# Kernel tuning notes

Hardware: AMD Instinct MI355X
Metric: run time of the kernel (lower is better)

Reference implementation:

```python
import jax, jax.numpy as jnp
import numpy as np


def _conv1x1(x, w, b):
    # x: [B,C,H,W], w: [O,C], b: [O] -> [B,O,H,W]
    return jnp.einsum('bchw,oc->bohw', x, w) + b[None, :, None, None]


def setup_inputs() -> dict:
    key = jax.random.key(0)
    ks = jax.random.split(key, 5)
    B, C, H, W = 4, 256, 64, 64
    C2 = C // 2
    scale = 0.02  # keep attention logits in a sane range
    return {
        'x': jax.random.normal(ks[0], (B, C, H, W), dtype=jnp.float32),
        'w_theta': jax.random.normal(ks[1], (C2, C), dtype=jnp.float32) * scale,
        'b_theta': jnp.zeros((C2,), dtype=jnp.float32),
        'w_phi': jax.random.normal(ks[2], (C2, C), dtype=jnp.float32) * scale,
        'b_phi': jnp.zeros((C2,), dtype=jnp.float32),
        'w_g': jax.random.normal(ks[3], (C2, C), dtype=jnp.float32) * scale,
        'b_g': jnp.zeros((C2,), dtype=jnp.float32),
        'w_out': jax.random.normal(ks[4], (C, C2), dtype=jnp.float32) * scale,
        'b_out': jnp.zeros((C,), dtype=jnp.float32),
    }


def reference(x, w_theta, b_theta, w_phi, b_phi, w_g, b_g, w_out, b_out):
    B, C, H, W = x.shape
    C2 = C // 2
    N = H * W
    theta = _conv1x1(x, w_theta, b_theta).reshape(B, C2, N)  # [B,C2,N]
    phi = _conv1x1(x, w_phi, b_phi).reshape(B, C2, N)        # [B,C2,N]
    g = _conv1x1(x, w_g, b_g).reshape(B, C2, N)              # [B,C2,N]
    # non-local attention: scores[b,m,n] = theta[b,:,m] . phi[b,:,n]
    scores = jnp.einsum('bcm,bcn->bmn', theta, phi)          # [B,N,N]
    attn = jax.nn.softmax(scores, axis=-1)                   # [B,N,N]
    # output = g @ attn^T : out[b,c,m] = sum_n g[b,c,n] * attn[b,m,n]
    out = jnp.einsum('bcn,bmn->bcm', g, attn)                # [B,C2,N]
    out = out.reshape(B, C2, H, W)
    return x + _conv1x1(out, w_out, b_out)
```

## Files before the change

### kernel.cpp

```cpp
#include <hip/hip_runtime.h>
#include <hip/hip_bf16.h>

#define B_  4
#define C_  256
#define C2_ 128
#define N_  4096
#define LOG2E 1.4426950408889634f

typedef unsigned short u16;
typedef __attribute__((ext_vector_type(8))) short bf16x8;
typedef __attribute__((ext_vector_type(4))) float f32x4;

static __device__ __forceinline__ u16 f2bf(float f) {
    return __builtin_bit_cast(u16, __float2bfloat16(f));
}
static __device__ __forceinline__ float bf2f(u16 u) {
    return __bfloat162float(__builtin_bit_cast(__hip_bfloat16, u));
}
static __device__ __forceinline__ bf16x8 cvt8(const float* p) {
    u16 t[8];
#pragma unroll
    for (int j = 0; j < 8; ++j) t[j] = f2bf(p[j]);
    return *(const bf16x8*)t;
}

__global__ __launch_bounds__(256, 2) void projx_kernel(
    const float* __restrict__ x,
    const float* __restrict__ wt, const float* __restrict__ wp,
    const float* __restrict__ wg,
    const float* __restrict__ b_theta, const float* __restrict__ b_phi,
    const float* __restrict__ b_g,
    u16* __restrict__ Q, u16* __restrict__ K, u16* __restrict__ V) {
    __shared__ __align__(16) u16 XTs[64][264];
    __shared__ __align__(16) u16 Ws[64][264];
    u16 (*Vt)[72] = (u16(*)[72])XTs;

    int bid = blockIdx.x;
    int b   = bid / (N_ / 64);
    int n0  = (bid % (N_ / 64)) * 64;
    int tid = threadIdx.x;
    int wave = tid >> 6, lane = tid & 63, quad = (lane >> 4) & 3, l16 = lane & 15;

#pragma unroll
    for (int it = 0; it < 8; ++it) {
        int idx = it * 256 + tid;
        int q = idx & 15, p = idx >> 4;
        const float* r0 = x + ((size_t)b * C_ + 2 * p) * N_ + n0 + 4 * q;
        float4 v0 = *(const float4*)r0;
        float4 v1 = *(const float4*)(r0 + N_);
        const float* f0 = (const float*)&v0;
        const float* f1 = (const float*)&v1;
#pragma unroll
        for (int j = 0; j < 4; ++j) {
            unsigned pk = (unsigned)f2bf(f0[j]) | ((unsigned)f2bf(f1[j]) << 16);
            *(unsigned*)&XTs[4 * q + j][2 * p] = pk;
        }
    }
    __syncthreads();

    bf16x8 af[8];
#pragma unroll
    for (int ks = 0; ks < 8; ++ks)
        af[ks] = *(const bf16x8*)&XTs[wave * 16 + l16][ks * 32 + quad * 8];
    __syncthreads();

    const float* wms[3]    = { wt, wp, wg };
    const float* biases[3] = { b_theta, b_phi, b_g };

#pragma unroll
    for (int mat = 0; mat < 3; ++mat) {
        const float* wm = wms[mat];
        const float* bias = biases[mat];
#pragma unroll
        for (int h = 0; h < 2; ++h) {
#pragma unroll
            for (int it = 0; it < 8; ++it) {
                int idx = it * 256 + tid;
                int row = idx >> 5, c8 = (idx & 31) * 8;
                const float* src = wm + (size_t)(h * 64 + row) * C_ + c8;
                float w8[8];
                *(float4*)&w8[0] = *(const float4*)src;
                *(float4*)&w8[4] = *(const float4*)(src + 4);
                bf16x8 v = cvt8(w8);
                *(bf16x8*)&Ws[row][c8] = v;
            }
            __syncthreads();

            f32x4 acc[4];
#pragma unroll
            for (int i = 0; i < 4; ++i) acc[i] = (f32x4){0.f, 0.f, 0.f, 0.f};
#pragma unroll
            for (int ct = 0; ct < 4; ++ct)
#pragma unroll
                for (int ks = 0; ks < 8; ++ks) {
                    bf16x8 bf = *(const bf16x8*)&Ws[ct * 16 + l16][ks * 32 + quad * 8];
                    acc[ct] = __builtin_amdgcn_mfma_f32_16x16x32_bf16(
                        af[ks], bf, acc[ct], 0, 0, 0);
                }

            if (mat < 2) {
                u16* dst = mat == 0 ? Q : K;
                float sc = mat == 0 ? LOG2E : 1.0f;
#pragma unroll
                for (int ct = 0; ct < 4; ++ct) {
                    int c2 = h * 64 + ct * 16 + l16;
                    float bb = bias[c2];
#pragma unroll
                    for (int r = 0; r < 4; ++r) {
                        int n = n0 + wave * 16 + quad * 4 + r;
                        dst[((size_t)b * N_ + n) * C2_ + c2] =
                            f2bf((acc[ct][r] + bb) * sc);
                    }
                }
            } else {
#pragma unroll
                for (int ct = 0; ct < 4; ++ct) {
                    int c2 = h * 64 + ct * 16 + l16;
                    float bb = bias[c2];
#pragma unroll
                    for (int r = 0; r < 4; ++r)
                        Vt[c2][wave * 16 + quad * 4 + r] = f2bf(acc[ct][r] + bb);
                }
            }
            __syncthreads();
        }
    }

#pragma unroll
    for (int it = 0; it < 4; ++it) {
        int idx = it * 256 + tid;
        int row = idx >> 3, n8 = (idx & 7) * 8;
        *(uint4*)(V + ((size_t)b * C2_ + row) * N_ + n0 + n8) =
            *(const uint4*)&Vt[row][n8];
    }
}

__global__ __launch_bounds__(256, 2) void attn_kernel(
    const u16* __restrict__ Q, const u16* __restrict__ K,
    const u16* __restrict__ V, u16* __restrict__ AO,
    u16* __restrict__ Opb, float* __restrict__ lsum, int nsplit) {
    const int BM = 128, BN = 64, D = C2_;
    const int per = B_ * (N_ / BM);
    int s    = blockIdx.x / per;
    int r0   = blockIdx.x % per;
    int b    = r0 / (N_ / BM);
    int m0   = (r0 % (N_ / BM)) * BM;
    int tid  = threadIdx.x;
    int wave = tid >> 6, lane = tid & 63, quad = (lane >> 4) & 3, l16 = lane & 15;

    __shared__ __align__(16) u16 Ks[BN][D + 8];
    __shared__ __align__(16) u16 Vs[D][BN + 8];
    __shared__ __align__(16) u16 Psb[4][32][BN + 8];
    u16* Ps = &Psb[wave][0][0];

    bf16x8 qf[2][4];
#pragma unroll
    for (int ms = 0; ms < 2; ++ms) {
        const u16* qp = Q + ((size_t)b * N_ + m0 + wave * 32 + ms * 16 + l16) * D;
#pragma unroll
        for (int kk = 0; kk < 4; ++kk)
            qf[ms][kk] = *(const bf16x8*)(qp + kk * 32 + quad * 8);
    }

    float l_r[2][4] = {{0.f, 0.f, 0.f, 0.f}, {0.f, 0.f, 0.f, 0.f}};
    f32x4 o_acc[2][8];
#pragma unroll
    for (int ms = 0; ms < 2; ++ms)
#pragma unroll
        for (int i = 0; i < 8; ++i) o_acc[ms][i] = (f32x4){0.f, 0.f, 0.f, 0.f};

    const int tiles = N_ / BN;
    const int base = tiles / nsplit, rem = tiles % nsplit;
    const int t0 = s * base + (s < rem ? s : rem);
    const int cnt = base + (s < rem ? 1 : 0);
    const int nt0 = t0 * BN, nt1 = (t0 + cnt) * BN;

    for (int nt = nt0; nt < nt1; nt += BN) {
        const u16* kp = K + ((size_t)b * N_ + nt) * D;
#pragma unroll
        for (int it = 0; it < 4; ++it) {
            int idx = it * 256 + tid;
            int row = idx >> 4, col = (idx & 15) * 8;
            *(uint4*)&Ks[row][col] = *(const uint4*)(kp + row * D + col);
        }
#pragma unroll
        for (int it = 0; it < 4; ++it) {
            int idx = it * 256 + tid;
            int row = idx >> 3, col = (idx & 7) * 8;
            *(uint4*)&Vs[row][col] =
                *(const uint4*)(V + ((size_t)b * C2_ + row) * N_ + nt + col);
        }
        __syncthreads();

        f32x4 sc[2][4];
#pragma unroll
        for (int nn = 0; nn < 4; ++nn) {
            f32x4 a0 = (f32x4){0.f, 0.f, 0.f, 0.f};
            f32x4 a1 = (f32x4){0.f, 0.f, 0.f, 0.f};
#pragma unroll
            for (int kk = 0; kk < 4; ++kk) {
                bf16x8 kf = *(const bf16x8*)&Ks[nn * 16 + l16][kk * 32 + quad * 8];
                a0 = __builtin_amdgcn_mfma_f32_16x16x32_bf16(qf[0][kk], kf, a0, 0, 0, 0);
                a1 = __builtin_amdgcn_mfma_f32_16x16x32_bf16(qf[1][kk], kf, a1, 0, 0, 0);
            }
            sc[0][nn] = a0;
            sc[1][nn] = a1;
        }

#pragma unroll
        for (int ms = 0; ms < 2; ++ms)
#pragma unroll
            for (int nn = 0; nn < 4; ++nn)
#pragma unroll
                for (int r = 0; r < 4; ++r) {
                    float p = __builtin_amdgcn_exp2f(sc[ms][nn][r]);
                    l_r[ms][r] += p;
                    Ps[(ms * 16 + quad * 4 + r) * (BN + 8) + nn * 16 + l16] = f2bf(p);
                }

#pragma unroll
        for (int ks = 0; ks < 2; ++ks) {
            bf16x8 pf0 = *(const bf16x8*)&Ps[(l16) * (BN + 8) + ks * 32 + quad * 8];
            bf16x8 pf1 = *(const bf16x8*)&Ps[(16 + l16) * (BN + 8) + ks * 32 + quad * 8];
#pragma unroll
            for (int cs = 0; cs < 8; ++cs) {
                bf16x8 vf = *(const bf16x8*)&Vs[cs * 16 + l16][ks * 32 + quad * 8];
                o_acc[0][cs] = __builtin_amdgcn_mfma_f32_16x16x32_bf16(pf0, vf, o_acc[0][cs], 0, 0, 0);
                o_acc[1][cs] = __builtin_amdgcn_mfma_f32_16x16x32_bf16(pf1, vf, o_acc[1][cs], 0, 0, 0);
            }
        }
        __syncthreads();
    }

#pragma unroll
    for (int ms = 0; ms < 2; ++ms)
#pragma unroll
        for (int r = 0; r < 4; ++r) {
            l_r[ms][r] += __shfl_xor(l_r[ms][r], 1);
            l_r[ms][r] += __shfl_xor(l_r[ms][r], 2);
            l_r[ms][r] += __shfl_xor(l_r[ms][r], 4);
            l_r[ms][r] += __shfl_xor(l_r[ms][r], 8);
        }

    if (Opb) {
#pragma unroll
        for (int ms = 0; ms < 2; ++ms) {
#pragma unroll
            for (int cs = 0; cs < 8; ++cs)
#pragma unroll
                for (int r = 0; r < 4; ++r) {
                    size_t row = (size_t)s * (B_ * N_) + (size_t)b * N_ +
                                 m0 + wave * 32 + ms * 16 + quad * 4 + r;
                    Opb[row * C2_ + cs * 16 + l16] = f2bf(o_acc[ms][cs][r]);
                }
            if (l16 == 0)
#pragma unroll
                for (int r = 0; r < 4; ++r) {
                    size_t row = (size_t)s * (B_ * N_) + (size_t)b * N_ +
                                 m0 + wave * 32 + ms * 16 + quad * 4 + r;
                    lsum[row] = l_r[ms][r];
                }
        }
    } else {
#pragma unroll
        for (int ms = 0; ms < 2; ++ms)
#pragma unroll
            for (int cs = 0; cs < 8; ++cs)
#pragma unroll
                for (int r = 0; r < 4; ++r) {
                    float v = o_acc[ms][cs][r] / l_r[ms][r];
                    AO[((size_t)b * N_ + m0 + wave * 32 + ms * 16 + quad * 4 + r) * C2_ +
                       cs * 16 + l16] = f2bf(v);
                }
    }
}

__global__ __launch_bounds__(256) void outproj_kernel(
    const float* __restrict__ x, const u16* __restrict__ Opb,
    const float* __restrict__ lsum, const u16* __restrict__ AO,
    const float* __restrict__ w_out, const float* __restrict__ b_out,
    float* __restrict__ y, int nsplit) {
    __shared__ __align__(16) u16 As[64][C2_ + 8];
    __shared__ __align__(16) u16 Ws2[64][C2_ + 8];
    __shared__ float Ls[64];
    int bid = blockIdx.x;
    int per_b = (C_ / 64) * (N_ / 64);
    int b   = bid / per_b;
    int rem = bid % per_b;
    int c0  = (rem / (N_ / 64)) * 64;
    int n0  = (rem % (N_ / 64)) * 64;
    int tid = threadIdx.x;
    int wave = tid >> 6, lane = tid & 63, quad = (lane >> 4) & 3, l16 = lane & 15;

#pragma unroll
    for (int it = 0; it < 4; ++it) {
        int idx = it * 256 + tid;
        int row = idx >> 4, c8 = (idx & 15) * 8;
        const float* src = w_out + (size_t)(c0 + row) * C2_ + c8;
        float w8[8];
        *(float4*)&w8[0] = *(const float4*)src;
        *(float4*)&w8[4] = *(const float4*)(src + 4);
        bf16x8 v = cvt8(w8);
        *(bf16x8*)&Ws2[row][c8] = v;
    }

    if (nsplit > 1) {
        if (tid < 64) {
            float L = 0.f;
            for (int s = 0; s < nsplit; ++s)
                L += lsum[(size_t)s * (B_ * N_) + (size_t)b * N_ + n0 + tid];
            Ls[tid] = 1.f / L;
        }
        __syncthreads();
#pragma unroll
        for (int it = 0; it < 4; ++it) {
            int idx = it * 256 + tid;
            int n = idx >> 4, c8 = (idx & 15) * 8;
            float a[8] = {0.f, 0.f, 0.f, 0.f, 0.f, 0.f, 0.f, 0.f};
            for (int s = 0; s < nsplit; ++s) {
                const u16* op = Opb +
                    ((size_t)s * (B_ * N_) + (size_t)b * N_ + n0 + n) * C2_ + c8;
                uint4 raw = *(const uint4*)op;
                const u16* rp = (const u16*)&raw;
#pragma unroll
                for (int j = 0; j < 8; ++j) a[j] += bf2f(rp[j]);
            }
            float inv = Ls[n];
            u16 o[8];
#pragma unroll
            for (int j = 0; j < 8; ++j) o[j] = f2bf(a[j] * inv);
            *(uint4*)&As[n][c8] = *(const uint4*)o;
        }
    } else {
#pragma unroll
        for (int it = 0; it < 4; ++it) {
            int idx = it * 256 + tid;
            int n = idx >> 4, c8 = (idx & 15) * 8;
            *(uint4*)&As[n][c8] =
                *(const uint4*)(AO + ((size_t)b * N_ + n0 + n) * C2_ + c8);
        }
    }
    __syncthreads();

    bf16x8 af[4];
#pragma unroll
    for (int kk = 0; kk < 4; ++kk)
        af[kk] = *(const bf16x8*)&Ws2[wave * 16 + l16][kk * 32 + quad * 8];

    f32x4 acc[4];
#pragma unroll
    for (int i = 0; i < 4; ++i) acc[i] = (f32x4){0.f, 0.f, 0.f, 0.f};

#pragma unroll
    for (int nn = 0; nn < 4; ++nn)
#pragma unroll
        for (int kk = 0; kk < 4; ++kk) {
            bf16x8 bf = *(const bf16x8*)&As[nn * 16 + l16][kk * 32 + quad * 8];
            acc[nn] = __builtin_amdgcn_mfma_f32_16x16x32_bf16(af[kk], bf, acc[nn], 0, 0, 0);
        }

    int cw = c0 + wave * 16;
    float bo[4];
#pragma unroll
    for (int r = 0; r < 4; ++r) bo[r] = b_out[cw + quad * 4 + r];

#pragma unroll
    for (int nn = 0; nn < 4; ++nn)
#pragma unroll
        for (int r = 0; r < 4; ++r) {
            int c = cw + quad * 4 + r;
            size_t off = ((size_t)b * C_ + c) * N_ + n0 + nn * 16 + l16;
            y[off] = x[off] + bo[r] + acc[nn][r];
        }
}

extern "C" void kernel_launch(void* const* d_in, const int* in_sizes, int n_in,
                              void* d_out, int out_size, void* d_ws, size_t ws_size,
                              hipStream_t stream) {
    const float* x       = (const float*)d_in[0];
    const float* w_theta = (const float*)d_in[1];
    const float* b_theta = (const float*)d_in[2];
    const float* w_phi   = (const float*)d_in[3];
    const float* b_phi   = (const float*)d_in[4];
    const float* w_g     = (const float*)d_in[5];
    const float* b_g     = (const float*)d_in[6];
    const float* w_out   = (const float*)d_in[7];
    const float* b_out   = (const float*)d_in[8];
    float* y = (float*)d_out;

    const size_t SZ = (size_t)B_ * N_ * C2_;
    u16* Q = (u16*)d_ws;
    u16* K = Q + SZ;
    u16* V = K + SZ;
    char* dyn = (char*)(V + SZ);
    size_t fixedB = 3 * SZ * 2;

    size_t perS = SZ * 2 + (size_t)B_ * N_ * 4;

    int S;
    if      (ws_size >= fixedB + 4 * perS) S = 4;
    else if (ws_size >= fixedB + 2 * perS) S = 2;
    else                                   S = 1;

    u16*   AO  = (u16*)dyn;
    u16*   Opb = nullptr;
    float* ls  = nullptr;
    if (S > 1) {
        Opb = (u16*)dyn;
        ls  = (float*)(Opb + (size_t)S * SZ);
    }

    projx_kernel<<<B_ * (N_ / 64), 256, 0, stream>>>(
        x, w_theta, w_phi, w_g, b_theta, b_phi, b_g, Q, K, V);
    attn_kernel<<<B_ * (N_ / 128) * S, 256, 0, stream>>>(Q, K, V, AO, Opb, ls, S);
    outproj_kernel<<<B_ * (C_ / 64) * (N_ / 64), 256, 0, stream>>>(
        x, Opb, ls, AO, w_out, b_out, y, S);
}
```

Measured before the change: 154.7 us.

## Raise occupancy, reuse LDS for P, pad LDS strides, split projection grid

The projection kernel now splits the output channels across two blocks, doubling its grid. The attention kernel drops its separate P buffer by aliasing it onto the K tile behind an extra barrier, which shrinks LDS so launch bounds can rise to 4 blocks per CU. LDS rows get new padded strides and 8-element accesses are split into 4-element halves to avoid bank conflicts. The split count can go up to 8 when workspace allows. The risks are duplicated x loads and conversion in the projection, an extra barrier per tile in attention, and more partial-sum traffic at higher split counts.

Result: slower. 263.3 us (+70.2%).

```diff
diff --git a/kernel.cpp b/kernel.cpp
--- a/kernel.cpp
+++ b/kernel.cpp
@@ -9,6 +9,7 @@
 
 typedef unsigned short u16;
 typedef __attribute__((ext_vector_type(8))) short bf16x8;
+typedef __attribute__((ext_vector_type(4))) short s16x4;
 typedef __attribute__((ext_vector_type(4))) float f32x4;
 
 static __device__ __forceinline__ u16 f2bf(float f) {
@@ -23,6 +24,17 @@
     for (int j = 0; j < 8; ++j) t[j] = f2bf(p[j]);
     return *(const bf16x8*)t;
 }
+static __device__ __forceinline__ bf16x8 lds8(const u16* p) {
+    s16x4 lo = *(const s16x4*)p;
+    s16x4 hi = *(const s16x4*)(p + 4);
+    return __builtin_shufflevector(lo, hi, 0, 1, 2, 3, 4, 5, 6, 7);
+}
+static __device__ __forceinline__ void st8(u16* p, bf16x8 v) {
+    *(s16x4*)p       = __builtin_shufflevector(v, v, 0, 1, 2, 3);
+    *(s16x4*)(p + 4) = __builtin_shufflevector(v, v, 4, 5, 6, 7);
+}
+
+#define XW 268
 
 __global__ __launch_bounds__(256, 2) void projx_kernel(
     const float* __restrict__ x,
@@ -31,13 +43,15 @@
     const float* __restrict__ b_theta, const float* __restrict__ b_phi,
     const float* __restrict__ b_g,
     u16* __restrict__ Q, u16* __restrict__ K, u16* __restrict__ V) {
-    __shared__ __align__(16) u16 XTs[64][264];
-    __shared__ __align__(16) u16 Ws[64][264];
+    __shared__ __align__(16) u16 XTs[64][XW];
+    __shared__ __align__(16) u16 Ws[64][XW];
     u16 (*Vt)[72] = (u16(*)[72])XTs;
 
     int bid = blockIdx.x;
-    int b   = bid / (N_ / 64);
-    int n0  = (bid % (N_ / 64)) * 64;
+    int h   = bid >> 8;
+    int r2  = bid & 255;
+    int b   = r2 >> 6;
+    int n0  = (r2 & 63) * 64;
     int tid = threadIdx.x;
     int wave = tid >> 6, lane = tid & 63, quad = (lane >> 4) & 3, l16 = lane & 15;
 
@@ -61,7 +75,7 @@
     bf16x8 af[8];
 #pragma unroll
     for (int ks = 0; ks < 8; ++ks)
-        af[ks] = *(const bf16x8*)&XTs[wave * 16 + l16][ks * 32 + quad * 8];
+        af[ks] = lds8(&XTs[wave * 16 + l16][ks * 32 + quad * 8]);
     __syncthreads();
 
     const float* wms[3]    = { wt, wp, wg };
@@ -72,70 +86,71 @@
         const float* wm = wms[mat];
         const float* bias = biases[mat];
 #pragma unroll
-        for (int h = 0; h < 2; ++h) {
-#pragma unroll
-            for (int it = 0; it < 8; ++it) {
-                int idx = it * 256 + tid;
-                int row = idx >> 5, c8 = (idx & 31) * 8;
-                const float* src = wm + (size_t)(h * 64 + row) * C_ + c8;
-                float w8[8];
-                *(float4*)&w8[0] = *(const float4*)src;
-                *(float4*)&w8[4] = *(const float4*)(src + 4);
-                bf16x8 v = cvt8(w8);
-                *(bf16x8*)&Ws[row][c8] = v;
-            }
-            __syncthreads();
-
-            f32x4 acc[4];
-#pragma unroll
-            for (int i = 0; i < 4; ++i) acc[i] = (f32x4){0.f, 0.f, 0.f, 0.f};
-#pragma unroll
-            for (int ct = 0; ct < 4; ++ct)
-#pragma unroll
-                for (int ks = 0; ks < 8; ++ks) {
-                    bf16x8 bf = *(const bf16x8*)&Ws[ct * 16 + l16][ks * 32 + quad * 8];
-                    acc[ct] = __builtin_amdgcn_mfma_f32_16x16x32_bf16(
-                        af[ks], bf, acc[ct], 0, 0, 0);
-                }
-
-            if (mat < 2) {
-                u16* dst = mat == 0 ? Q : K;
-                float sc = mat == 0 ? LOG2E : 1.0f;
-#pragma unroll
-                for (int ct = 0; ct < 4; ++ct) {
-                    int c2 = h * 64 + ct * 16 + l16;
-                    float bb = bias[c2];
-#pragma unroll
-                    for (int r = 0; r < 4; ++r) {
-                        int n = n0 + wave * 16 + quad * 4 + r;
-                        dst[((size_t)b * N_ + n) * C2_ + c2] =
-                            f2bf((acc[ct][r] + bb) * sc);
-                    }
-                }
-            } else {
-#pragma unroll
-                for (int ct = 0; ct < 4; ++ct) {
-                    int c2 = h * 64 + ct * 16 + l16;
-                    float bb = bias[c2];
-#pragma unroll
-                    for (int r = 0; r < 4; ++r)
-                        Vt[c2][wave * 16 + quad * 4 + r] = f2bf(acc[ct][r] + bb);
-                }
-            }
-            __syncthreads();
-        }
-    }
-
-#pragma unroll
-    for (int it = 0; it < 4; ++it) {
+        for (int it = 0; it < 8; ++it) {
+            int idx = it * 256 + tid;
+            int row = idx >> 5, c8 = (idx & 31) * 8;
+            const float* src = wm + (size_t)(h * 64 + row) * C_ + c8;
+            float w8[8];
+            *(float4*)&w8[0] = *(const float4*)src;
+            *(float4*)&w8[4] = *(const float4*)(src + 4);
+            st8(&Ws[row][c8], cvt8(w8));
+        }
+        __syncthreads();
+
+        f32x4 acc[4];
+#pragma unroll
+        for (int i = 0; i < 4; ++i) acc[i] = (f32x4){0.f, 0.f, 0.f, 0.f};
+#pragma unroll
+        for (int ct = 0; ct < 4; ++ct)
+#pragma unroll
+            for (int ks = 0; ks < 8; ++ks) {
+                bf16x8 bf = lds8(&Ws[ct * 16 + l16][ks * 32 + quad * 8]);
+                acc[ct] = __builtin_amdgcn_mfma_f32_16x16x32_bf16(
+                    af[ks], bf, acc[ct], 0, 0, 0);
+            }
+
+        if (mat < 2) {
+            u16* dst = mat == 0 ? Q : K;
+            float scl = mat == 0 ? LOG2E : 1.0f;
+#pragma unroll
+            for (int ct = 0; ct < 4; ++ct) {
+                int c2 = h * 64 + ct * 16 + l16;
+                float bb = bias[c2];
+#pragma unroll
+                for (int r = 0; r < 4; ++r) {
+                    int n = n0 + wave * 16 + quad * 4 + r;
+                    dst[((size_t)b * N_ + n) * C2_ + c2] =
+                        f2bf((acc[ct][r] + bb) * scl);
+                }
+            }
+        } else {
+#pragma unroll
+            for (int ct = 0; ct < 4; ++ct) {
+                int c2 = h * 64 + ct * 16 + l16;
+                float bb = bias[c2];
+#pragma unroll
+                for (int r = 0; r < 4; ++r)
+                    Vt[ct * 16 + l16][wave * 16 + quad * 4 + r] =
+                        f2bf(acc[ct][r] + bb);
+            }
+        }
+        __syncthreads();
+    }
+
+#pragma unroll
+    for (int it = 0; it < 2; ++it) {
         int idx = it * 256 + tid;
         int row = idx >> 3, n8 = (idx & 7) * 8;
-        *(uint4*)(V + ((size_t)b * C2_ + row) * N_ + n0 + n8) =
+        *(uint4*)(V + ((size_t)b * C2_ + h * 64 + row) * N_ + n0 + n8) =
             *(const uint4*)&Vt[row][n8];
     }
 }
 
-__global__ __launch_bounds__(256, 2) void attn_kernel(
+#define KS_LD 140
+#define VS_LD 76
+#define PS_LD 68
+
+__global__ __launch_bounds__(256, 4) void attn_kernel(
     const u16* __restrict__ Q, const u16* __restrict__ K,
     const u16* __restrict__ V, u16* __restrict__ AO,
     u16* __restrict__ Opb, float* __restrict__ lsum, int nsplit) {
@@ -148,10 +163,9 @@
     int tid  = threadIdx.x;
     int wave = tid >> 6, lane = tid & 63, quad = (lane >> 4) & 3, l16 = lane & 15;
 
-    __shared__ __align__(16) u16 Ks[BN][D + 8];
-    __shared__ __align__(16) u16 Vs[D][BN + 8];
-    __shared__ __align__(16) u16 Psb[4][32][BN + 8];
-    u16* Ps = &Psb[wave][0][0];
+    __shared__ __align__(16) u16 Ks[BN][KS_LD];
+    __shared__ __align__(16) u16 Vs[C2_][VS_LD];
+    u16* Ps = &Ks[0][0] + wave * (32 * PS_LD);
 
     bf16x8 qf[2][4];
 #pragma unroll
@@ -181,14 +195,17 @@
         for (int it = 0; it < 4; ++it) {
             int idx = it * 256 + tid;
             int row = idx >> 4, col = (idx & 15) * 8;
-            *(uint4*)&Ks[row][col] = *(const uint4*)(kp + row * D + col);
+            uint4 raw = *(const uint4*)(kp + row * D + col);
+            *(uint2*)&Ks[row][col]     = make_uint2(raw.x, raw.y);
+            *(uint2*)&Ks[row][col + 4] = make_uint2(raw.z, raw.w);
         }
 #pragma unroll
         for (int it = 0; it < 4; ++it) {
             int idx = it * 256 + tid;
             int row = idx >> 3, col = (idx & 7) * 8;
-            *(uint4*)&Vs[row][col] =
-                *(const uint4*)(V + ((size_t)b * C2_ + row) * N_ + nt + col);
+            uint4 raw = *(const uint4*)(V + ((size_t)b * C2_ + row) * N_ + nt + col);
+            *(uint2*)&Vs[row][col]     = make_uint2(raw.x, raw.y);
+            *(uint2*)&Vs[row][col + 4] = make_uint2(raw.z, raw.w);
         }
         __syncthreads();
 
@@ -199,7 +216,7 @@
             f32x4 a1 = (f32x4){0.f, 0.f, 0.f, 0.f};
 #pragma unroll
             for (int kk = 0; kk < 4; ++kk) {
-                bf16x8 kf = *(const bf16x8*)&Ks[nn * 16 + l16][kk * 32 + quad * 8];
+                bf16x8 kf = lds8(&Ks[nn * 16 + l16][kk * 32 + quad * 8]);
                 a0 = __builtin_amdgcn_mfma_f32_16x16x32_bf16(qf[0][kk], kf, a0, 0, 0, 0);
                 a1 = __builtin_amdgcn_mfma_f32_16x16x32_bf16(qf[1][kk], kf, a1, 0, 0, 0);
             }
@@ -207,24 +224,42 @@
             sc[1][nn] = a1;
         }
 
+        unsigned pkd[2][4][2];
 #pragma unroll
         for (int ms = 0; ms < 2; ++ms)
 #pragma unroll
             for (int nn = 0; nn < 4; ++nn)
 #pragma unroll
-                for (int r = 0; r < 4; ++r) {
-                    float p = __builtin_amdgcn_exp2f(sc[ms][nn][r]);
-                    l_r[ms][r] += p;
-                    Ps[(ms * 16 + quad * 4 + r) * (BN + 8) + nn * 16 + l16] = f2bf(p);
+                for (int rp = 0; rp < 2; ++rp) {
+                    float p0 = __builtin_amdgcn_exp2f(sc[ms][nn][2 * rp]);
+                    float p1 = __builtin_amdgcn_exp2f(sc[ms][nn][2 * rp + 1]);
+                    l_r[ms][2 * rp]     += p0;
+                    l_r[ms][2 * rp + 1] += p1;
+                    pkd[ms][nn][rp] =
+                        (unsigned)f2bf(p0) | ((unsigned)f2bf(p1) << 16);
+                }
+
+        __syncthreads();
+
+#pragma unroll
+        for (int ms = 0; ms < 2; ++ms)
+#pragma unroll
+            for (int nn = 0; nn < 4; ++nn)
+#pragma unroll
+                for (int rp = 0; rp < 2; ++rp) {
+                    unsigned v = pkd[ms][nn][rp];
+                    int rb = (ms * 16 + quad * 4 + 2 * rp) * PS_LD + nn * 16 + l16;
+                    Ps[rb]         = (u16)v;
+                    Ps[rb + PS_LD] = (u16)(v >> 16);
                 }
 
 #pragma unroll
         for (int ks = 0; ks < 2; ++ks) {
-            bf16x8 pf0 = *(const bf16x8*)&Ps[(l16) * (BN + 8) + ks * 32 + quad * 8];
-            bf16x8 pf1 = *(const bf16x8*)&Ps[(16 + l16) * (BN + 8) + ks * 32 + quad * 8];
+            bf16x8 pf0 = lds8(Ps + l16 * PS_LD + ks * 32 + quad * 8);
+            bf16x8 pf1 = lds8(Ps + (16 + l16) * PS_LD + ks * 32 + quad * 8);
 #pragma unroll
             for (int cs = 0; cs < 8; ++cs) {
-                bf16x8 vf = *(const bf16x8*)&Vs[cs * 16 + l16][ks * 32 + quad * 8];
+                bf16x8 vf = lds8(&Vs[cs * 16 + l16][ks * 32 + quad * 8]);
                 o_acc[0][cs] = __builtin_amdgcn_mfma_f32_16x16x32_bf16(pf0, vf, o_acc[0][cs], 0, 0, 0);
                 o_acc[1][cs] = __builtin_amdgcn_mfma_f32_16x16x32_bf16(pf1, vf, o_acc[1][cs], 0, 0, 0);
             }
@@ -275,13 +310,15 @@
     }
 }
 
-__global__ __launch_bounds__(256) void outproj_kernel(
+#define OW 140
+
+__global__ __launch_bounds__(256, 4) void outproj_kernel(
     const float* __restrict__ x, const u16* __restrict__ Opb,
     const float* __restrict__ lsum, const u16* __restrict__ AO,
     const float* __restrict__ w_out, const float* __restrict__ b_out,
     float* __restrict__ y, int nsplit) {
-    __shared__ __align__(16) u16 As[64][C2_ + 8];
-    __shared__ __align__(16) u16 Ws2[64][C2_ + 8];
+    __shared__ __align__(16) u16 As[64][OW];
+    __shared__ __align__(16) u16 Ws2[64][OW];
     __shared__ float Ls[64];
     int bid = blockIdx.x;
     int per_b = (C_ / 64) * (N_ / 64);
@@ -300,8 +337,7 @@
         float w8[8];
         *(float4*)&w8[0] = *(const float4*)src;
         *(float4*)&w8[4] = *(const float4*)(src + 4);
-        bf16x8 v = cvt8(w8);
-        *(bf16x8*)&Ws2[row][c8] = v;
+        st8(&Ws2[row][c8], cvt8(w8));
     }
 
     if (nsplit > 1) {
@@ -329,15 +365,16 @@
             u16 o[8];
 #pragma unroll
             for (int j = 0; j < 8; ++j) o[j] = f2bf(a[j] * inv);
-            *(uint4*)&As[n][c8] = *(const uint4*)o;
+            st8(&As[n][c8], *(const bf16x8*)o);
         }
     } else {
 #pragma unroll
         for (int it = 0; it < 4; ++it) {
             int idx = it * 256 + tid;
             int n = idx >> 4, c8 = (idx & 15) * 8;
-            *(uint4*)&As[n][c8] =
-                *(const uint4*)(AO + ((size_t)b * N_ + n0 + n) * C2_ + c8);
+            uint4 raw = *(const uint4*)(AO + ((size_t)b * N_ + n0 + n) * C2_ + c8);
+            *(uint2*)&As[n][c8]     = make_uint2(raw.x, raw.y);
+            *(uint2*)&As[n][c8 + 4] = make_uint2(raw.z, raw.w);
         }
     }
     __syncthreads();
@@ -345,7 +382,7 @@
     bf16x8 af[4];
 #pragma unroll
     for (int kk = 0; kk < 4; ++kk)
-        af[kk] = *(const bf16x8*)&Ws2[wave * 16 + l16][kk * 32 + quad * 8];
+        af[kk] = lds8(&Ws2[wave * 16 + l16][kk * 32 + quad * 8]);
 
     f32x4 acc[4];
 #pragma unroll
@@ -355,7 +392,7 @@
     for (int nn = 0; nn < 4; ++nn)
 #pragma unroll
         for (int kk = 0; kk < 4; ++kk) {
-            bf16x8 bf = *(const bf16x8*)&As[nn * 16 + l16][kk * 32 + quad * 8];
+            bf16x8 bf = lds8(&As[nn * 16 + l16][kk * 32 + quad * 8]);
             acc[nn] = __builtin_amdgcn_mfma_f32_16x16x32_bf16(af[kk], bf, acc[nn], 0, 0, 0);
         }
 
@@ -398,7 +435,8 @@
     size_t perS = SZ * 2 + (size_t)B_ * N_ * 4;
 
     int S;
-    if      (ws_size >= fixedB + 4 * perS) S = 4;
+    if      (ws_size >= fixedB + 8 * perS) S = 8;
+    else if (ws_size >= fixedB + 4 * perS) S = 4;
     else if (ws_size >= fixedB + 2 * perS) S = 2;
     else                                   S = 1;
 
@@ -410,7 +448,7 @@
         ls  = (float*)(Opb + (size_t)S * SZ);
     }
 
-    projx_kernel<<<B_ * (N_ / 64), 256, 0, stream>>>(
+    projx_kernel<<<B_ * (N_ / 64) * 2, 256, 0, stream>>>(
         x, w_theta, w_phi, w_g, b_theta, b_phi, b_g, Q, K, V);
     attn_kernel<<<B_ * (N_ / 128) * S, 256, 0, stream>>>(Q, K, V, AO, Opb, ls, S);
     outproj_kernel<<<B_ * (C_ / 64) * (N_ / 64), 256, 0, stream>>>(
```
